# Optimization experiments

Hardware: AMD Instinct MI355X
Metric: run time of the kernel (lower is better)

## Reference

```python
import jax, jax.numpy as jnp
import numpy as np

B, S, D = 8, 1024, 1024
H = 2048            # expert hidden dim
E = 8               # num experts
TOP_K = 2
D_NOISE = 256
TEMP = 1.0


def setup_inputs() -> dict:
    key = jax.random.key(0)
    ks = jax.random.split(key, 8)
    return {
        "x": jax.random.normal(ks[0], (B, S, D), dtype=jnp.float32),
        "noise_clock_emb": jax.random.normal(ks[1], (B, D_NOISE), dtype=jnp.float32),
        # router weight [D_noise, E] (xavier-ish scale)
        "route_weight": jax.random.normal(ks[2], (D_NOISE, E), dtype=jnp.float32) * (1.0 / np.sqrt(D_NOISE)),
        # stacked expert params; torch Linear y = x @ W.T + b, stored here pre-transposed
        "fc_in_w": jax.random.normal(ks[3], (E, D, 2 * H), dtype=jnp.float32) * 0.02,
        "fc_in_b": jax.random.normal(ks[4], (E, 2 * H), dtype=jnp.float32) * 0.02,
        "fc_out_w": jax.random.normal(ks[5], (E, H, D), dtype=jnp.float32) * 0.02,
        "fc_out_b": jax.random.normal(ks[6], (E, D), dtype=jnp.float32) * 0.02,
    }


def reference(x, noise_clock_emb, route_weight, fc_in_w, fc_in_b, fc_out_w, fc_out_b):
    # ---- router: P = softmax(phi(sigma) @ W_R / T) ----
    logits = (noise_clock_emb @ route_weight) / TEMP            # [B, E]
    probs = jax.nn.softmax(logits, axis=-1)
    topk_weights, topk_indices = jax.lax.top_k(probs, TOP_K)    # [B, K]
    topk_weights = topk_weights / jnp.clip(
        topk_weights.sum(axis=-1, keepdims=True), 1e-8)
    # dense per-(batch, expert) mixing coefficient, identical to the
    # masked accumulation in the torch loop
    coeff = jnp.einsum("bke,bk->be",
                       jax.nn.one_hot(topk_indices, E, dtype=x.dtype),
                       topk_weights)                             # [B, E]

    # ---- all experts densely over the full batch (matches original math) ----
    h = jnp.einsum("bsd,edh->ebsh", x, fc_in_w) + fc_in_b[:, None, None, :]
    value, gate = jnp.split(h, 2, axis=-1)                       # [E,B,S,H] each
    hidden = value * jax.nn.silu(gate)
    mixed = jnp.einsum("ebsh,ehd,be->bsd", hidden, fc_out_w, coeff)
    mixed = mixed + jnp.einsum("be,ed->bd", coeff, fc_out_b)[:, None, :]
    return mixed, logits, probs, topk_indices, topk_weights
```

## Files before the change

kernel.cpp:

```cpp
#include <hip/hip_runtime.h>
#include <stdint.h>

#define B_ 8
#define S_ 1024
#define D_ 1024
#define H_ 2048
#define E_ 8
#define DN_ 256

typedef unsigned char u8;
typedef float f32x4 __attribute__((ext_vector_type(4)));
typedef long long ll;

__device__ __forceinline__ u8 f2f8(float f) {
  return (u8)(__builtin_amdgcn_cvt_pk_fp8_f32(f, f, 0, false) & 0xff);
}
__device__ __forceinline__ unsigned int pk4f8(float a, float b, float c, float d) {
  int w = __builtin_amdgcn_cvt_pk_fp8_f32(a, b, 0, false);
  w = __builtin_amdgcn_cvt_pk_fp8_f32(c, d, w, true);
  return (unsigned int)w;
}

__device__ __forceinline__ void gll16(const void* g, void* l) {
  __builtin_amdgcn_global_load_lds(
      (__attribute__((address_space(1))) void*)g,
      (__attribute__((address_space(3))) void*)l, 16, 0, 0);
}

__device__ __forceinline__ int swz(int r) { return (r & 3) ^ ((r >> 2) & 1); }

template <int R, int C>
__device__ __forceinline__ void transpose_body(const float* __restrict__ ip,
                                               u8* __restrict__ op,
                                               int bx, int by, int t,
                                               u8 (&tile)[64][72]) {
  const int r0 = by * 64, c0 = bx * 64;
  const int rr = t >> 4;
  const int c4 = t & 15;
#pragma unroll
  for (int i = 0; i < 4; ++i) {
    const int r = rr + i * 16;
    float4 v = *(const float4*)(ip + (size_t)(r0 + r) * C + c0 + c4 * 4);
    tile[c4 * 4 + 0][r] = f2f8(v.x);
    tile[c4 * 4 + 1][r] = f2f8(v.y);
    tile[c4 * 4 + 2][r] = f2f8(v.z);
    tile[c4 * 4 + 3][r] = f2f8(v.w);
  }
  __syncthreads();
#pragma unroll
  for (int i = 0; i < 4; ++i) {
    const int c = rr + i * 16;
    unsigned int w = *(const unsigned int*)&tile[c][c4 * 4];
    *(unsigned int*)(op + (size_t)(c0 + c) * R + r0 + c4 * 4) = w;
  }
}

#define NCAST (B_ * S_ * D_ / 1024)
#define NT1 ((2 * H_ / 64) * (D_ / 64) * E_)
#define NT2 ((D_ / 64) * (H_ / 64) * E_)

__global__ void __launch_bounds__(256) prep_kernel(
    const float* __restrict__ x, const float* __restrict__ noise,
    const float* __restrict__ rw, const float* __restrict__ fiw,
    const float* __restrict__ fow,
    float* __restrict__ out_logits, float* __restrict__ out_probs,
    float* __restrict__ out_idx, float* __restrict__ out_w,
    int* __restrict__ ws_idx, float* __restrict__ ws_w,
    unsigned int* __restrict__ xq, u8* __restrict__ wtin,
    u8* __restrict__ wtout) {
  __shared__ __align__(16) u8 tile[64][72];
  const int t = threadIdx.x;
  int bid = blockIdx.x;

  if (bid == 0) {
    float* sl = (float*)&tile[0][0];
    float* sp = sl + 64;
    {
      const int pair = t >> 2, sub = t & 3;
      const int b = pair >> 3, e = pair & 7;
      float acc = 0.f;
      const int d0 = sub * 64;
      for (int d = d0; d < d0 + 64; ++d)
        acc += noise[b * DN_ + d] * rw[d * E_ + e];
      acc += __shfl_xor(acc, 1);
      acc += __shfl_xor(acc, 2);
      if (sub == 0) sl[pair] = acc;
    }
    __syncthreads();
    if (t < 64) {
      const int b = t >> 3;
      float L = sl[t];
      out_logits[t] = L;
      float m = -1e30f;
      for (int j = 0; j < 8; ++j) m = fmaxf(m, sl[b * 8 + j]);
      float s = 0.f;
      for (int j = 0; j < 8; ++j) s += __expf(sl[b * 8 + j] - m);
      float p = __expf(L - m) / s;
      out_probs[t] = p;
      sp[t] = p;
    }
    __syncthreads();
    if (t < 64 && (t & 7) == 0) {
      const int b = t >> 3;
      int a1 = 0; float v1 = sp[b * 8];
      for (int j = 1; j < 8; ++j) { float v = sp[b * 8 + j]; if (v > v1) { v1 = v; a1 = j; } }
      int a2 = -1; float v2 = -1e30f;
      for (int j = 0; j < 8; ++j) {
        if (j == a1) continue;
        float v = sp[b * 8 + j]; if (v > v2) { v2 = v; a2 = j; }
      }
      float sum = fmaxf(v1 + v2, 1e-8f);
      float w1 = v1 / sum, w2 = v2 / sum;
      out_idx[b * 2] = (float)a1; out_idx[b * 2 + 1] = (float)a2;
      out_w[b * 2] = w1; out_w[b * 2 + 1] = w2;
      ws_idx[b * 2] = a1; ws_idx[b * 2 + 1] = a2;
      ws_w[b * 2] = w1; ws_w[b * 2 + 1] = w2;
    }
    return;
  }
  bid -= 1;
  if (bid < NCAST) {
    const size_t i = (size_t)bid * 256 + t;
    float4 v = *((const float4*)x + i);
    xq[i] = pk4f8(v.x, v.y, v.z, v.w);
    return;
  }
  bid -= NCAST;
  if (bid < NT1) {
    const int bx = bid & 63, by = (bid >> 6) & 15, e = bid >> 10;
    transpose_body<D_, 2 * H_>(fiw + (size_t)e * D_ * 2 * H_,
                               wtin + (size_t)e * D_ * 2 * H_, bx, by, t, tile);
    return;
  }
  bid -= NT1;
  {
    const int bx = bid & 15, by = (bid >> 4) & 31, e = bid >> 9;
    transpose_body<H_, D_>(fow + (size_t)e * H_ * D_,
                           wtout + (size_t)e * H_ * D_, bx, by, t, tile);
  }
}

__global__ void __launch_bounds__(256, 4) gemm1_kernel(
    const u8* __restrict__ xq,
    const u8* __restrict__ wtin,
    const float* __restrict__ bin,
    const int* __restrict__ ws_idx, const float* __restrict__ ws_w,
    u8* __restrict__ hid)
{
  const int nt = blockIdx.x;
  const int mt = blockIdx.y;
  const int z  = blockIdx.z;
  const int b  = z >> 1;
  const int e  = ws_idx[z] & 7;
  const float csc = ws_w[z];

  __shared__ u8 As[128 * 64];
  __shared__ u8 Bs[128 * 64];

  const int t = threadIdx.x;
  const int wave = t >> 6, lane = t & 63;
  const int wm = wave >> 1, wn = wave & 1;
  const int lm = lane & 15, lq = lane >> 4;
  const int lrow4 = lane >> 2;
  const int kq = ((lane & 3) ^ swz(lrow4)) * 16;
  const int fsw = swz(lm);
  const int p0 = lq >> 1, fb = (lq & 1) * 8;

  const u8* Ab  = xq + (size_t)b * (S_ * D_) + (size_t)mt * 128 * D_;
  const u8* Bvb = wtin + (size_t)e * (2 * H_ * D_) + (size_t)nt * 64 * D_;
  const u8* Bgb = Bvb + (size_t)H_ * D_;

  const f32x4 vz = {0.f, 0.f, 0.f, 0.f};
  f32x4 accv[4][2], accg[4][2];
#pragma unroll
  for (int i = 0; i < 4; ++i)
#pragma unroll
    for (int j = 0; j < 2; ++j) { accv[i][j] = vz; accg[i][j] = vz; }

  for (int kt = 0; kt < D_ / 64; ++kt) {
    const int k0 = kt * 64 + kq;
    gll16(Ab + (size_t)(wave * 16 + lrow4) * D_ + k0, (char*)As + wave * 1024);
    gll16(Ab + (size_t)((wave + 4) * 16 + lrow4) * D_ + k0, (char*)As + (wave + 4) * 1024);
    gll16(Bvb + (size_t)(wave * 16 + lrow4) * D_ + k0, (char*)Bs + wave * 1024);
    gll16(Bgb + (size_t)(wave * 16 + lrow4) * D_ + k0, (char*)Bs + 4096 + wave * 1024);
    __syncthreads();
    ll af[4][2], bvf[2][2], bgf[2][2];
#pragma unroll
    for (int h = 0; h < 2; ++h) {
      const int pw = ((h * 2 + p0) ^ fsw) * 16 + fb;
#pragma unroll
      for (int i = 0; i < 4; ++i)
        af[i][h] = *(const ll*)(As + (wm * 64 + i * 16 + lm) * 64 + pw);
#pragma unroll
      for (int j = 0; j < 2; ++j) {
        bvf[j][h] = *(const ll*)(Bs + (wn * 32 + j * 16 + lm) * 64 + pw);
        bgf[j][h] = *(const ll*)(Bs + (64 + wn * 32 + j * 16 + lm) * 64 + pw);
      }
    }
#pragma unroll
    for (int h = 0; h < 2; ++h)
#pragma unroll
      for (int i = 0; i < 4; ++i)
#pragma unroll
        for (int j = 0; j < 2; ++j) {
          accv[i][j] = __builtin_amdgcn_mfma_f32_16x16x32_fp8_fp8(af[i][h], bvf[j][h], accv[i][j], 0, 0, 0);
          accg[i][j] = __builtin_amdgcn_mfma_f32_16x16x32_fp8_fp8(af[i][h], bgf[j][h], accg[i][j], 0, 0, 0);
        }
    __syncthreads();
  }

  u8* hb = hid + (size_t)z * (S_ * H_);
  const int row0 = mt * 128 + wm * 64;
  const int col0 = nt * 64 + wn * 32;
#pragma unroll
  for (int j = 0; j < 2; ++j) {
    const int col = col0 + j * 16 + lm;
    const float bvx = bin[e * 2 * H_ + col];
    const float bgx = bin[e * 2 * H_ + H_ + col];
#pragma unroll
    for (int i = 0; i < 4; ++i) {
#pragma unroll
      for (int r = 0; r < 4; ++r) {
        const int srow = row0 + i * 16 + lq * 4 + r;
        float v = accv[i][j][r] + bvx;
        float g = accg[i][j][r] + bgx;
        float hv = v * g / (1.f + __expf(-g)) * csc;
        hb[(size_t)srow * H_ + col] = f2f8(hv);
      }
    }
  }
}

__global__ void __launch_bounds__(256, 4) gemm2_kernel(
    const u8* __restrict__ hid,
    const u8* __restrict__ wtout,
    const float* __restrict__ bout,
    const int* __restrict__ ws_idx, const float* __restrict__ ws_w,
    float* __restrict__ out)
{
  const int nt = blockIdx.x;
  const int mt = blockIdx.y;
  const int b  = blockIdx.z;

  __shared__ u8 As[128 * 64];
  __shared__ u8 Bs[64 * 64];

  const int t = threadIdx.x;
  const int wave = t >> 6, lane = t & 63;
  const int wm = wave >> 1, wn = wave & 1;
  const int lm = lane & 15, lq = lane >> 4;
  const int lrow4 = lane >> 2;
  const int kq = ((lane & 3) ^ swz(lrow4)) * 16;
  const int fsw = swz(lm);
  const int p0 = lq >> 1, fb = (lq & 1) * 8;

  const f32x4 vz = {0.f, 0.f, 0.f, 0.f};
  f32x4 acc[4][2];
#pragma unroll
  for (int i = 0; i < 4; ++i)
#pragma unroll
    for (int j = 0; j < 2; ++j) acc[i][j] = vz;

  for (int slot = 0; slot < 2; ++slot) {
    const int e = ws_idx[b * 2 + slot] & 7;
    const u8* Ab = hid + ((size_t)(b * 2 + slot) * S_ + mt * 128) * H_;
    const u8* Bb = wtout + ((size_t)e * D_ + nt * 64) * H_;
    for (int kt = 0; kt < H_ / 64; ++kt) {
      const int k0 = kt * 64 + kq;
      gll16(Ab + (size_t)(wave * 16 + lrow4) * H_ + k0, (char*)As + wave * 1024);
      gll16(Ab + (size_t)((wave + 4) * 16 + lrow4) * H_ + k0, (char*)As + (wave + 4) * 1024);
      gll16(Bb + (size_t)(wave * 16 + lrow4) * H_ + k0, (char*)Bs + wave * 1024);
      __syncthreads();
      ll af[4][2], bf[2][2];
#pragma unroll
      for (int h = 0; h < 2; ++h) {
        const int pw = ((h * 2 + p0) ^ fsw) * 16 + fb;
#pragma unroll
        for (int i = 0; i < 4; ++i)
          af[i][h] = *(const ll*)(As + (wm * 64 + i * 16 + lm) * 64 + pw);
#pragma unroll
        for (int j = 0; j < 2; ++j)
          bf[j][h] = *(const ll*)(Bs + (wn * 32 + j * 16 + lm) * 64 + pw);
      }
#pragma unroll
      for (int h = 0; h < 2; ++h)
#pragma unroll
        for (int i = 0; i < 4; ++i)
#pragma unroll
          for (int j = 0; j < 2; ++j)
            acc[i][j] = __builtin_amdgcn_mfma_f32_16x16x32_fp8_fp8(af[i][h], bf[j][h], acc[i][j], 0, 0, 0);
      __syncthreads();
    }
  }

  const int e0 = ws_idx[b * 2] & 7, e1 = ws_idx[b * 2 + 1] & 7;
  const float c0 = ws_w[b * 2], c1 = ws_w[b * 2 + 1];
  float* ob = out + (size_t)b * (S_ * D_);
  const int row0 = mt * 128 + wm * 64;
  const int col0 = nt * 64 + wn * 32;
#pragma unroll
  for (int j = 0; j < 2; ++j) {
    const int col = col0 + j * 16 + lm;
    const float bias = c0 * bout[e0 * D_ + col] + c1 * bout[e1 * D_ + col];
#pragma unroll
    for (int i = 0; i < 4; ++i)
#pragma unroll
      for (int r = 0; r < 4; ++r)
        ob[(size_t)(row0 + i * 16 + lq * 4 + r) * D_ + col] = acc[i][j][r] + bias;
  }
}

extern "C" void kernel_launch(void* const* d_in, const int* in_sizes, int n_in,
                              void* d_out, int out_size, void* d_ws, size_t ws_size,
                              hipStream_t stream) {
  const float* x     = (const float*)d_in[0];
  const float* noise = (const float*)d_in[1];
  const float* rw    = (const float*)d_in[2];
  const float* fiw   = (const float*)d_in[3];
  const float* fib   = (const float*)d_in[4];
  const float* fow   = (const float*)d_in[5];
  const float* fob   = (const float*)d_in[6];
  float* out = (float*)d_out;

  char* ws = (char*)d_ws;
  int*   ws_idx = (int*)ws;
  float* ws_w   = (float*)(ws + 64);
  u8* xq    = (u8*)(ws + 256);
  u8* wtin  = xq + (size_t)B_ * S_ * D_;
  u8* wtout = wtin + (size_t)E_ * 2 * H_ * D_;
  u8* hid   = wtout + (size_t)E_ * D_ * H_;

  float* out_mixed  = out;
  float* out_logits = out + (size_t)B_ * S_ * D_;
  float* out_probs  = out_logits + B_ * E_;
  float* out_idx    = out_probs + B_ * E_;
  float* out_w      = out_idx + B_ * 2;

  prep_kernel<<<1 + NCAST + NT1 + NT2, 256, 0, stream>>>(
      x, noise, rw, fiw, fow, out_logits, out_probs, out_idx, out_w,
      ws_idx, ws_w, (unsigned int*)xq, wtin, wtout);
  gemm1_kernel<<<dim3(32, 8, 16), 256, 0, stream>>>(xq, wtin, fib, ws_idx, ws_w, hid);
  gemm2_kernel<<<dim3(16, 8, 8), 256, 0, stream>>>(hid, wtout, fob, ws_idx, ws_w, out_mixed);
}
```

Baseline: 432.0 us.

## Double-buffer LDS tiles in both expert GEMMs to overlap loads with MFMA

Result: slower. 447.0 us (+3.5%).

```diff
diff --git a/kernel.cpp b/kernel.cpp
--- a/kernel.cpp
+++ b/kernel.cpp
@@ -154,8 +154,8 @@
   const int e  = ws_idx[z] & 7;
   const float csc = ws_w[z];
 
-  __shared__ u8 As[128 * 64];
-  __shared__ u8 Bs[128 * 64];
+  __shared__ u8 As[2][128 * 64];
+  __shared__ u8 Bs[2][128 * 64];
 
   const int t = threadIdx.x;
   const int wave = t >> 6, lane = t & 63;
@@ -170,6 +170,14 @@
   const u8* Bvb = wtin + (size_t)e * (2 * H_ * D_) + (size_t)nt * 64 * D_;
   const u8* Bgb = Bvb + (size_t)H_ * D_;
 
+  auto stage = [&](int bf, int kt) {
+    const int k0 = kt * 64 + kq;
+    gll16(Ab + (size_t)(wave * 16 + lrow4) * D_ + k0, (char*)As[bf] + wave * 1024);
+    gll16(Ab + (size_t)((wave + 4) * 16 + lrow4) * D_ + k0, (char*)As[bf] + (wave + 4) * 1024);
+    gll16(Bvb + (size_t)(wave * 16 + lrow4) * D_ + k0, (char*)Bs[bf] + wave * 1024);
+    gll16(Bgb + (size_t)(wave * 16 + lrow4) * D_ + k0, (char*)Bs[bf] + 4096 + wave * 1024);
+  };
+
   const f32x4 vz = {0.f, 0.f, 0.f, 0.f};
   f32x4 accv[4][2], accg[4][2];
 #pragma unroll
@@ -177,24 +185,25 @@
 #pragma unroll
     for (int j = 0; j < 2; ++j) { accv[i][j] = vz; accg[i][j] = vz; }
 
+  stage(0, 0);
+  __syncthreads();
+  int cur = 0;
+#pragma unroll 2
   for (int kt = 0; kt < D_ / 64; ++kt) {
-    const int k0 = kt * 64 + kq;
-    gll16(Ab + (size_t)(wave * 16 + lrow4) * D_ + k0, (char*)As + wave * 1024);
-    gll16(Ab + (size_t)((wave + 4) * 16 + lrow4) * D_ + k0, (char*)As + (wave + 4) * 1024);
-    gll16(Bvb + (size_t)(wave * 16 + lrow4) * D_ + k0, (char*)Bs + wave * 1024);
-    gll16(Bgb + (size_t)(wave * 16 + lrow4) * D_ + k0, (char*)Bs + 4096 + wave * 1024);
-    __syncthreads();
+    if (kt + 1 < D_ / 64) stage(cur ^ 1, kt + 1);
+    const u8* Asc = As[cur];
+    const u8* Bsc = Bs[cur];
     ll af[4][2], bvf[2][2], bgf[2][2];
 #pragma unroll
     for (int h = 0; h < 2; ++h) {
       const int pw = ((h * 2 + p0) ^ fsw) * 16 + fb;
 #pragma unroll
       for (int i = 0; i < 4; ++i)
-        af[i][h] = *(const ll*)(As + (wm * 64 + i * 16 + lm) * 64 + pw);
+        af[i][h] = *(const ll*)(Asc + (wm * 64 + i * 16 + lm) * 64 + pw);
 #pragma unroll
       for (int j = 0; j < 2; ++j) {
-        bvf[j][h] = *(const ll*)(Bs + (wn * 32 + j * 16 + lm) * 64 + pw);
-        bgf[j][h] = *(const ll*)(Bs + (64 + wn * 32 + j * 16 + lm) * 64 + pw);
+        bvf[j][h] = *(const ll*)(Bsc + (wn * 32 + j * 16 + lm) * 64 + pw);
+        bgf[j][h] = *(const ll*)(Bsc + (64 + wn * 32 + j * 16 + lm) * 64 + pw);
       }
     }
 #pragma unroll
@@ -207,6 +216,7 @@
           accg[i][j] = __builtin_amdgcn_mfma_f32_16x16x32_fp8_fp8(af[i][h], bgf[j][h], accg[i][j], 0, 0, 0);
         }
     __syncthreads();
+    cur ^= 1;
   }
 
   u8* hb = hid + (size_t)z * (S_ * H_);
@@ -242,8 +252,8 @@
   const int mt = blockIdx.y;
   const int b  = blockIdx.z;
 
-  __shared__ u8 As[128 * 64];
-  __shared__ u8 Bs[64 * 64];
+  __shared__ u8 As[2][128 * 64];
+  __shared__ u8 Bs[2][64 * 64];
 
   const int t = threadIdx.x;
   const int wave = t >> 6, lane = t & 63;
@@ -254,6 +264,21 @@
   const int fsw = swz(lm);
   const int p0 = lq >> 1, fb = (lq & 1) * 8;
 
+  const int e0 = ws_idx[b * 2] & 7, e1 = ws_idx[b * 2 + 1] & 7;
+  const u8* Ab0 = hid + ((size_t)(b * 2 + 0) * S_ + mt * 128) * H_;
+  const u8* Ab1 = hid + ((size_t)(b * 2 + 1) * S_ + mt * 128) * H_;
+  const u8* Bb0 = wtout + ((size_t)e0 * D_ + nt * 64) * H_;
+  const u8* Bb1 = wtout + ((size_t)e1 * D_ + nt * 64) * H_;
+
+  auto stage = [&](int bf, int it) {
+    const u8* Ab = (it & 32) ? Ab1 : Ab0;
+    const u8* Bb = (it & 32) ? Bb1 : Bb0;
+    const int k0 = (it & 31) * 64 + kq;
+    gll16(Ab + (size_t)(wave * 16 + lrow4) * H_ + k0, (char*)As[bf] + wave * 1024);
+    gll16(Ab + (size_t)((wave + 4) * 16 + lrow4) * H_ + k0, (char*)As[bf] + (wave + 4) * 1024);
+    gll16(Bb + (size_t)(wave * 16 + lrow4) * H_ + k0, (char*)Bs[bf] + wave * 1024);
+  };
+
   const f32x4 vz = {0.f, 0.f, 0.f, 0.f};
   f32x4 acc[4][2];
 #pragma unroll
@@ -261,39 +286,36 @@
 #pragma unroll
     for (int j = 0; j < 2; ++j) acc[i][j] = vz;
 
-  for (int slot = 0; slot < 2; ++slot) {
-    const int e = ws_idx[b * 2 + slot] & 7;
-    const u8* Ab = hid + ((size_t)(b * 2 + slot) * S_ + mt * 128) * H_;
-    const u8* Bb = wtout + ((size_t)e * D_ + nt * 64) * H_;
-    for (int kt = 0; kt < H_ / 64; ++kt) {
-      const int k0 = kt * 64 + kq;
-      gll16(Ab + (size_t)(wave * 16 + lrow4) * H_ + k0, (char*)As + wave * 1024);
-      gll16(Ab + (size_t)((wave + 4) * 16 + lrow4) * H_ + k0, (char*)As + (wave + 4) * 1024);
-      gll16(Bb + (size_t)(wave * 16 + lrow4) * H_ + k0, (char*)Bs + wave * 1024);
-      __syncthreads();
-      ll af[4][2], bf[2][2];
-#pragma unroll
-      for (int h = 0; h < 2; ++h) {
-        const int pw = ((h * 2 + p0) ^ fsw) * 16 + fb;
-#pragma unroll
-        for (int i = 0; i < 4; ++i)
-          af[i][h] = *(const ll*)(As + (wm * 64 + i * 16 + lm) * 64 + pw);
+  stage(0, 0);
+  __syncthreads();
+  int cur = 0;
+#pragma unroll 2
+  for (int it = 0; it < 64; ++it) {
+    if (it + 1 < 64) stage(cur ^ 1, it + 1);
+    const u8* Asc = As[cur];
+    const u8* Bsc = Bs[cur];
+    ll af[4][2], bf[2][2];
+#pragma unroll
+    for (int h = 0; h < 2; ++h) {
+      const int pw = ((h * 2 + p0) ^ fsw) * 16 + fb;
+#pragma unroll
+      for (int i = 0; i < 4; ++i)
+        af[i][h] = *(const ll*)(Asc + (wm * 64 + i * 16 + lm) * 64 + pw);
+#pragma unroll
+      for (int j = 0; j < 2; ++j)
+        bf[j][h] = *(const ll*)(Bsc + (wn * 32 + j * 16 + lm) * 64 + pw);
+    }
+#pragma unroll
+    for (int h = 0; h < 2; ++h)
+#pragma unroll
+      for (int i = 0; i < 4; ++i)
 #pragma unroll
         for (int j = 0; j < 2; ++j)
-          bf[j][h] = *(const ll*)(Bs + (wn * 32 + j * 16 + lm) * 64 + pw);
-      }
-#pragma unroll
-      for (int h = 0; h < 2; ++h)
-#pragma unroll
-        for (int i = 0; i < 4; ++i)
-#pragma unroll
-          for (int j = 0; j < 2; ++j)
-            acc[i][j] = __builtin_amdgcn_mfma_f32_16x16x32_fp8_fp8(af[i][h], bf[j][h], acc[i][j], 0, 0, 0);
-      __syncthreads();
-    }
-  }
-
-  const int e0 = ws_idx[b * 2] & 7, e1 = ws_idx[b * 2 + 1] & 7;
+          acc[i][j] = __builtin_amdgcn_mfma_f32_16x16x32_fp8_fp8(af[i][h], bf[j][h], acc[i][j], 0, 0, 0);
+    __syncthreads();
+    cur ^= 1;
+  }
+
   const float c0 = ws_w[b * 2], c1 = ws_w[b * 2 + 1];
   float* ob = out + (size_t)b * (S_ * D_);
   const int row0 = mt * 128 + wm * 64;
```

## Double GEMM K-tile to 128 with 8-way swizzle and widen weight transpose

Applied to the files above, without the earlier changes.

Result: no change. 425.1 us (-1.6%).

```diff
diff --git a/kernel.cpp b/kernel.cpp
--- a/kernel.cpp
+++ b/kernel.cpp
@@ -9,16 +9,17 @@
 #define DN_ 256
 
 typedef unsigned char u8;
+typedef unsigned int u32;
 typedef float f32x4 __attribute__((ext_vector_type(4)));
 typedef long long ll;
 
 __device__ __forceinline__ u8 f2f8(float f) {
   return (u8)(__builtin_amdgcn_cvt_pk_fp8_f32(f, f, 0, false) & 0xff);
 }
-__device__ __forceinline__ unsigned int pk4f8(float a, float b, float c, float d) {
+__device__ __forceinline__ u32 pk4f8(float a, float b, float c, float d) {
   int w = __builtin_amdgcn_cvt_pk_fp8_f32(a, b, 0, false);
   w = __builtin_amdgcn_cvt_pk_fp8_f32(c, d, w, true);
-  return (unsigned int)w;
+  return (u32)w;
 }
 
 __device__ __forceinline__ void gll16(const void* g, void* l) {
@@ -27,37 +28,44 @@
       (__attribute__((address_space(3))) void*)l, 16, 0, 0);
 }
 
-__device__ __forceinline__ int swz(int r) { return (r & 3) ^ ((r >> 2) & 1); }
-
 template <int R, int C>
 __device__ __forceinline__ void transpose_body(const float* __restrict__ ip,
                                                u8* __restrict__ op,
                                                int bx, int by, int t,
-                                               u8 (&tile)[64][72]) {
-  const int r0 = by * 64, c0 = bx * 64;
-  const int rr = t >> 4;
-  const int c4 = t & 15;
-#pragma unroll
-  for (int i = 0; i < 4; ++i) {
-    const int r = rr + i * 16;
-    float4 v = *(const float4*)(ip + (size_t)(r0 + r) * C + c0 + c4 * 4);
-    tile[c4 * 4 + 0][r] = f2f8(v.x);
-    tile[c4 * 4 + 1][r] = f2f8(v.y);
-    tile[c4 * 4 + 2][r] = f2f8(v.z);
-    tile[c4 * 4 + 3][r] = f2f8(v.w);
+                                               u32 (&tl)[64][65]) {
+  const int r0 = by * 256, c0 = bx * 64;
+  const int rg16 = t >> 4;
+  const int cg = t & 15;
+#pragma unroll
+  for (int p = 0; p < 4; ++p) {
+    const int rq = p * 16 + rg16;
+    const float* q = ip + (size_t)(r0 + rq * 4) * C + c0 + cg * 4;
+    float4 v0 = *(const float4*)(q);
+    float4 v1 = *(const float4*)(q + C);
+    float4 v2 = *(const float4*)(q + 2 * C);
+    float4 v3 = *(const float4*)(q + 3 * C);
+    tl[cg * 4 + 0][rq] = pk4f8(v0.x, v1.x, v2.x, v3.x);
+    tl[cg * 4 + 1][rq] = pk4f8(v0.y, v1.y, v2.y, v3.y);
+    tl[cg * 4 + 2][rq] = pk4f8(v0.z, v1.z, v2.z, v3.z);
+    tl[cg * 4 + 3][rq] = pk4f8(v0.w, v1.w, v2.w, v3.w);
   }
   __syncthreads();
-#pragma unroll
-  for (int i = 0; i < 4; ++i) {
-    const int c = rr + i * 16;
-    unsigned int w = *(const unsigned int*)&tile[c][c4 * 4];
-    *(unsigned int*)(op + (size_t)(c0 + c) * R + r0 + c4 * 4) = w;
+  const int ch = t & 15;
+#pragma unroll
+  for (int p = 0; p < 4; ++p) {
+    const int c = p * 16 + (t >> 4);
+    uint4 w;
+    w.x = tl[c][ch * 4 + 0];
+    w.y = tl[c][ch * 4 + 1];
+    w.z = tl[c][ch * 4 + 2];
+    w.w = tl[c][ch * 4 + 3];
+    *(uint4*)(op + (size_t)(c0 + c) * R + r0 + ch * 16) = w;
   }
 }
 
 #define NCAST (B_ * S_ * D_ / 1024)
-#define NT1 ((2 * H_ / 64) * (D_ / 64) * E_)
-#define NT2 ((D_ / 64) * (H_ / 64) * E_)
+#define NT1 ((2 * H_ / 64) * (D_ / 256) * E_)
+#define NT2 ((D_ / 64) * (H_ / 256) * E_)
 
 __global__ void __launch_bounds__(256) prep_kernel(
     const float* __restrict__ x, const float* __restrict__ noise,
@@ -66,9 +74,9 @@
     float* __restrict__ out_logits, float* __restrict__ out_probs,
     float* __restrict__ out_idx, float* __restrict__ out_w,
     int* __restrict__ ws_idx, float* __restrict__ ws_w,
-    unsigned int* __restrict__ xq, u8* __restrict__ wtin,
+    u32* __restrict__ xq, u8* __restrict__ wtin,
     u8* __restrict__ wtout) {
-  __shared__ __align__(16) u8 tile[64][72];
+  __shared__ __align__(16) u32 tile[64][65];
   const int t = threadIdx.x;
   int bid = blockIdx.x;
 
@@ -127,14 +135,14 @@
   }
   bid -= NCAST;
   if (bid < NT1) {
-    const int bx = bid & 63, by = (bid >> 6) & 15, e = bid >> 10;
+    const int bx = bid & 63, by = (bid >> 6) & 3, e = bid >> 8;
     transpose_body<D_, 2 * H_>(fiw + (size_t)e * D_ * 2 * H_,
                                wtin + (size_t)e * D_ * 2 * H_, bx, by, t, tile);
     return;
   }
   bid -= NT1;
   {
-    const int bx = bid & 15, by = (bid >> 4) & 31, e = bid >> 9;
+    const int bx = bid & 15, by = (bid >> 4) & 7, e = bid >> 7;
     transpose_body<H_, D_>(fow + (size_t)e * H_ * D_,
                            wtout + (size_t)e * H_ * D_, bx, by, t, tile);
   }
@@ -154,16 +162,16 @@
   const int e  = ws_idx[z] & 7;
   const float csc = ws_w[z];
 
-  __shared__ u8 As[128 * 64];
-  __shared__ u8 Bs[128 * 64];
+  __shared__ u8 As[128 * 128];
+  __shared__ u8 Bs[128 * 128];
 
   const int t = threadIdx.x;
   const int wave = t >> 6, lane = t & 63;
   const int wm = wave >> 1, wn = wave & 1;
   const int lm = lane & 15, lq = lane >> 4;
-  const int lrow4 = lane >> 2;
-  const int kq = ((lane & 3) ^ swz(lrow4)) * 16;
-  const int fsw = swz(lm);
+  const int lrow8 = lane >> 3;
+  const int kq = ((lane & 7) ^ lrow8) * 16;
+  const int fsw = lm & 7;
   const int p0 = lq >> 1, fb = (lq & 1) * 8;
 
   const u8* Ab  = xq + (size_t)b * (S_ * D_) + (size_t)mt * 128 * D_;
@@ -177,35 +185,42 @@
 #pragma unroll
     for (int j = 0; j < 2; ++j) { accv[i][j] = vz; accg[i][j] = vz; }
 
-  for (int kt = 0; kt < D_ / 64; ++kt) {
-    const int k0 = kt * 64 + kq;
-    gll16(Ab + (size_t)(wave * 16 + lrow4) * D_ + k0, (char*)As + wave * 1024);
-    gll16(Ab + (size_t)((wave + 4) * 16 + lrow4) * D_ + k0, (char*)As + (wave + 4) * 1024);
-    gll16(Bvb + (size_t)(wave * 16 + lrow4) * D_ + k0, (char*)Bs + wave * 1024);
-    gll16(Bgb + (size_t)(wave * 16 + lrow4) * D_ + k0, (char*)Bs + 4096 + wave * 1024);
-    __syncthreads();
-    ll af[4][2], bvf[2][2], bgf[2][2];
-#pragma unroll
-    for (int h = 0; h < 2; ++h) {
-      const int pw = ((h * 2 + p0) ^ fsw) * 16 + fb;
-#pragma unroll
-      for (int i = 0; i < 4; ++i)
-        af[i][h] = *(const ll*)(As + (wm * 64 + i * 16 + lm) * 64 + pw);
-#pragma unroll
-      for (int j = 0; j < 2; ++j) {
-        bvf[j][h] = *(const ll*)(Bs + (wn * 32 + j * 16 + lm) * 64 + pw);
-        bgf[j][h] = *(const ll*)(Bs + (64 + wn * 32 + j * 16 + lm) * 64 + pw);
+  for (int kt = 0; kt < D_ / 128; ++kt) {
+    const int k0 = kt * 128 + kq;
+    gll16(Ab + (size_t)(wave * 8 + lrow8) * D_ + k0, (char*)As + wave * 1024);
+    gll16(Ab + (size_t)((wave + 4) * 8 + lrow8) * D_ + k0, (char*)As + (wave + 4) * 1024);
+    gll16(Ab + (size_t)((wave + 8) * 8 + lrow8) * D_ + k0, (char*)As + (wave + 8) * 1024);
+    gll16(Ab + (size_t)((wave + 12) * 8 + lrow8) * D_ + k0, (char*)As + (wave + 12) * 1024);
+    gll16(Bvb + (size_t)(wave * 8 + lrow8) * D_ + k0, (char*)Bs + wave * 1024);
+    gll16(Bvb + (size_t)((wave + 4) * 8 + lrow8) * D_ + k0, (char*)Bs + (wave + 4) * 1024);
+    gll16(Bgb + (size_t)(wave * 8 + lrow8) * D_ + k0, (char*)Bs + (8 + wave) * 1024);
+    gll16(Bgb + (size_t)((wave + 4) * 8 + lrow8) * D_ + k0, (char*)Bs + (12 + wave) * 1024);
+    __syncthreads();
+#pragma unroll
+    for (int hg = 0; hg < 2; ++hg) {
+      ll af[4][2], bvf[2][2], bgf[2][2];
+#pragma unroll
+      for (int h2 = 0; h2 < 2; ++h2) {
+        const int pw = ((((hg * 2 + h2) * 2 + p0) ^ fsw)) * 16 + fb;
+#pragma unroll
+        for (int i = 0; i < 4; ++i)
+          af[i][h2] = *(const ll*)(As + (wm * 64 + i * 16 + lm) * 128 + pw);
+#pragma unroll
+        for (int j = 0; j < 2; ++j) {
+          bvf[j][h2] = *(const ll*)(Bs + (wn * 32 + j * 16 + lm) * 128 + pw);
+          bgf[j][h2] = *(const ll*)(Bs + (64 + wn * 32 + j * 16 + lm) * 128 + pw);
+        }
       }
-    }
-#pragma unroll
-    for (int h = 0; h < 2; ++h)
-#pragma unroll
-      for (int i = 0; i < 4; ++i)
-#pragma unroll
-        for (int j = 0; j < 2; ++j) {
-          accv[i][j] = __builtin_amdgcn_mfma_f32_16x16x32_fp8_fp8(af[i][h], bvf[j][h], accv[i][j], 0, 0, 0);
-          accg[i][j] = __builtin_amdgcn_mfma_f32_16x16x32_fp8_fp8(af[i][h], bgf[j][h], accg[i][j], 0, 0, 0);
-        }
+#pragma unroll
+      for (int h2 = 0; h2 < 2; ++h2)
+#pragma unroll
+        for (int i = 0; i < 4; ++i)
+#pragma unroll
+          for (int j = 0; j < 2; ++j) {
+            accv[i][j] = __builtin_amdgcn_mfma_f32_16x16x32_fp8_fp8(af[i][h2], bvf[j][h2], accv[i][j], 0, 0, 0);
+            accg[i][j] = __builtin_amdgcn_mfma_f32_16x16x32_fp8_fp8(af[i][h2], bgf[j][h2], accg[i][j], 0, 0, 0);
+          }
+    }
     __syncthreads();
   }
 
@@ -242,17 +257,23 @@
   const int mt = blockIdx.y;
   const int b  = blockIdx.z;
 
-  __shared__ u8 As[128 * 64];
-  __shared__ u8 Bs[64 * 64];
+  __shared__ u8 As[128 * 128];
+  __shared__ u8 Bs[64 * 128];
 
   const int t = threadIdx.x;
   const int wave = t >> 6, lane = t & 63;
   const int wm = wave >> 1, wn = wave & 1;
   const int lm = lane & 15, lq = lane >> 4;
-  const int lrow4 = lane >> 2;
-  const int kq = ((lane & 3) ^ swz(lrow4)) * 16;
-  const int fsw = swz(lm);
+  const int lrow8 = lane >> 3;
+  const int kq = ((lane & 7) ^ lrow8) * 16;
+  const int fsw = lm & 7;
   const int p0 = lq >> 1, fb = (lq & 1) * 8;
+
+  const int e0 = ws_idx[b * 2] & 7, e1 = ws_idx[b * 2 + 1] & 7;
+  const u8* Ab0 = hid + ((size_t)(b * 2 + 0) * S_ + mt * 128) * H_;
+  const u8* Ab1 = hid + ((size_t)(b * 2 + 1) * S_ + mt * 128) * H_;
+  const u8* Bb0 = wtout + ((size_t)e0 * D_ + nt * 64) * H_;
+  const u8* Bb1 = wtout + ((size_t)e1 * D_ + nt * 64) * H_;
 
   const f32x4 vz = {0.f, 0.f, 0.f, 0.f};
   f32x4 acc[4][2];
@@ -261,39 +282,41 @@
 #pragma unroll
     for (int j = 0; j < 2; ++j) acc[i][j] = vz;
 
-  for (int slot = 0; slot < 2; ++slot) {
-    const int e = ws_idx[b * 2 + slot] & 7;
-    const u8* Ab = hid + ((size_t)(b * 2 + slot) * S_ + mt * 128) * H_;
-    const u8* Bb = wtout + ((size_t)e * D_ + nt * 64) * H_;
-    for (int kt = 0; kt < H_ / 64; ++kt) {
-      const int k0 = kt * 64 + kq;
-      gll16(Ab + (size_t)(wave * 16 + lrow4) * H_ + k0, (char*)As + wave * 1024);
-      gll16(Ab + (size_t)((wave + 4) * 16 + lrow4) * H_ + k0, (char*)As + (wave + 4) * 1024);
-      gll16(Bb + (size_t)(wave * 16 + lrow4) * H_ + k0, (char*)Bs + wave * 1024);
-      __syncthreads();
+  for (int it = 0; it < 32; ++it) {
+    const u8* Ab = (it & 16) ? Ab1 : Ab0;
+    const u8* Bb = (it & 16) ? Bb1 : Bb0;
+    const int k0 = (it & 15) * 128 + kq;
+    gll16(Ab + (size_t)(wave * 8 + lrow8) * H_ + k0, (char*)As + wave * 1024);
+    gll16(Ab + (size_t)((wave + 4) * 8 + lrow8) * H_ + k0, (char*)As + (wave + 4) * 1024);
+    gll16(Ab + (size_t)((wave + 8) * 8 + lrow8) * H_ + k0, (char*)As + (wave + 8) * 1024);
+    gll16(Ab + (size_t)((wave + 12) * 8 + lrow8) * H_ + k0, (char*)As + (wave + 12) * 1024);
+    gll16(Bb + (size_t)(wave * 8 + lrow8) * H_ + k0, (char*)Bs + wave * 1024);
+    gll16(Bb + (size_t)((wave + 4) * 8 + lrow8) * H_ + k0, (char*)Bs + (wave + 4) * 1024);
+    __syncthreads();
+#pragma unroll
+    for (int hg = 0; hg < 2; ++hg) {
       ll af[4][2], bf[2][2];
 #pragma unroll
-      for (int h = 0; h < 2; ++h) {
-        const int pw = ((h * 2 + p0) ^ fsw) * 16 + fb;
+      for (int h2 = 0; h2 < 2; ++h2) {
+        const int pw = ((((hg * 2 + h2) * 2 + p0) ^ fsw)) * 16 + fb;
 #pragma unroll
         for (int i = 0; i < 4; ++i)
-          af[i][h] = *(const ll*)(As + (wm * 64 + i * 16 + lm) * 64 + pw);
+          af[i][h2] = *(const ll*)(As + (wm * 64 + i * 16 + lm) * 128 + pw);
 #pragma unroll
         for (int j = 0; j < 2; ++j)
-          bf[j][h] = *(const ll*)(Bs + (wn * 32 + j * 16 + lm) * 64 + pw);
+          bf[j][h2] = *(const ll*)(Bs + (wn * 32 + j * 16 + lm) * 128 + pw);
       }
 #pragma unroll
-      for (int h = 0; h < 2; ++h)
+      for (int h2 = 0; h2 < 2; ++h2)
 #pragma unroll
         for (int i = 0; i < 4; ++i)
 #pragma unroll
           for (int j = 0; j < 2; ++j)
-            acc[i][j] = __builtin_amdgcn_mfma_f32_16x16x32_fp8_fp8(af[i][h], bf[j][h], acc[i][j], 0, 0, 0);
-      __syncthreads();
-    }
-  }
-
-  const int e0 = ws_idx[b * 2] & 7, e1 = ws_idx[b * 2 + 1] & 7;
+            acc[i][j] = __builtin_amdgcn_mfma_f32_16x16x32_fp8_fp8(af[i][h2], bf[j][h2], acc[i][j], 0, 0, 0);
+    }
+    __syncthreads();
+  }
+
   const float c0 = ws_w[b * 2], c1 = ws_w[b * 2 + 1];
   float* ob = out + (size_t)b * (S_ * D_);
   const int row0 = mt * 128 + wm * 64;
@@ -338,7 +361,7 @@
 
   prep_kernel<<<1 + NCAST + NT1 + NT2, 256, 0, stream>>>(
       x, noise, rw, fiw, fow, out_logits, out_probs, out_idx, out_w,
-      ws_idx, ws_w, (unsigned int*)xq, wtin, wtout);
+      ws_idx, ws_w, (u32*)xq, wtin, wtout);
   gemm1_kernel<<<dim3(32, 8, 16), 256, 0, stream>>>(xq, wtin, fib, ws_idx, ws_w, hid);
   gemm2_kernel<<<dim3(16, 8, 8), 256, 0, stream>>>(hid, wtout, fob, ws_idx, ws_w, out_mixed);
 }
```
